# Kernel optimization log

Hardware: AMD Instinct MI355X
Metric: run time of the kernel (lower is better)

The kernel has to match this reference:

```python
import jax, jax.numpy as jnp
import numpy as np

F, H, D, A, B = 500, 2000, 64, 64, 4096


def setup_inputs() -> dict:
    key = jax.random.key(0)
    ks = jax.random.split(key, 6)
    values = jax.random.normal(ks[0], (B, F), dtype=jnp.float32)
    feat_emb = jax.random.normal(ks[1], (F, D), dtype=jnp.float32) * 0.02
    hid_emb = jax.random.normal(ks[2], (H, D), dtype=jnp.float32) * 0.02
    Ww = jax.random.normal(ks[3], (2 * D, A), dtype=jnp.float32) * (1.0 / np.sqrt(2 * D))
    bw = jnp.zeros((A,), dtype=jnp.float32)
    Wu = jax.random.normal(ks[4], (A, 1), dtype=jnp.float32) * (1.0 / np.sqrt(A))
    mask = jax.random.bernoulli(ks[5], 0.1, (F, F + H, 1))
    return {"values": values, "feat_emb": feat_emb, "hid_emb": hid_emb,
            "Ww": Ww, "bw": bw, "Wu": Wu, "mask": mask}


def reference(values, feat_emb, hid_emb, Ww, bw, Wu, mask):
    d = feat_emb.shape[1]
    # full embedding matrix: concat(feature, hidden) -> [F+H, d]
    full = jnp.concatenate([feat_emb, hid_emb], axis=0)
    # Dense(tanh) on concat([feat_emb tiled, full tiled], axis=2) == split-weight form:
    # avoids materializing the [F, F+H, 2d] concat tensor (same math).
    W1, W2 = Ww[:d], Ww[d:]
    pre_f = feat_emb @ W1          # [F, A]
    pre_w = full @ W2              # [F+H, A]
    h = jnp.tanh(pre_f[:, None, :] + pre_w[None, :, :] + bw)  # [F, F+H, A]
    score = h @ Wu                 # [F, F+H, 1]
    # masked exp-normalize (not a stable softmax: original uses raw exp)
    score = jnp.where(mask, jnp.exp(score), 0.0)
    ssum = jnp.sum(score, axis=1, keepdims=True)        # [F, 1, 1]
    ssum = jnp.where(ssum == 0, 1.0, ssum)
    attn = score / ssum                                  # [F, F+H, 1]
    context = jnp.sum(attn * full[None, :, :], axis=1)   # [F, d]
    return values @ context                              # [B, d]
```

## Files before the change

### kernel.cpp

```cpp
#include <hip/hip_runtime.h>
#include <cstdint>
#include <cstddef>

#define F_N 500
#define H_N 2000
#define JN  2500
#define D_N 64
#define A_N 64
#define B_N 4096

#define SPLIT  2
#define JCHUNK 1250

__global__ __launch_bounds__(256) void k_pre(
    const float* __restrict__ feat, const float* __restrict__ hid,
    const float* __restrict__ Ww,   const float* __restrict__ bw,
    float* __restrict__ pre_f, float* __restrict__ pre_w)
{
    const int lane = threadIdx.x & 63;
    const int wave = threadIdx.x >> 6;
    int row = blockIdx.x * 4 + wave;
    row = __builtin_amdgcn_readfirstlane(row);
    if (row >= F_N + JN) return;

    const float* emb;
    const float* W;
    float*       outp;
    float acc0, acc1 = 0.0f;

    if (row < F_N) {
        emb  = feat + (size_t)row * D_N;
        W    = Ww;
        outp = pre_f + (size_t)row * A_N;
        acc0 = bw[lane];
    } else {
        const int j = row - F_N;
        emb  = (j < F_N) ? (feat + (size_t)j * D_N)
                         : (hid + (size_t)(j - F_N) * D_N);
        W    = Ww + D_N * A_N;
        outp = pre_w + (size_t)j * A_N;
        acc0 = 0.0f;
    }

    #pragma unroll
    for (int d = 0; d < D_N; d += 2) {
        acc0 = fmaf(emb[d],     W[(d    ) * A_N + lane], acc0);
        acc1 = fmaf(emb[d + 1], W[(d + 1) * A_N + lane], acc1);
    }
    outp[lane] = acc0 + acc1;
}

__global__ __launch_bounds__(256, 8) void k_attn(
    const float* __restrict__ feat, const float* __restrict__ hid,
    const float* __restrict__ pre_f, const float* __restrict__ pre_w,
    const float* __restrict__ Wu,   const void* __restrict__ mask,
    float* __restrict__ csum, float* __restrict__ esum)
{
    const int tid  = threadIdx.x;
    const int lane = tid & 63;
    const int wave = tid >> 6;
    const int i    = blockIdx.x >> 1;
    const int sub  = blockIdx.x & 1;
    const int jbase = sub * JCHUNK;

    __shared__ int   list[JCHUNK];
    __shared__ float earr[JCHUNK];
    __shared__ float s_ctx[4][64];
    __shared__ int   nact;

    if (tid == 0) nact = 0;
    __syncthreads();

    const uint32_t* mw = (const uint32_t*)mask;
    const uint32_t probe = mw[lane] | mw[64 + lane] | mw[128 + lane] | mw[192 + lane];
    const bool byteMode = (__ballot(probe > 1u) != 0ull);

    const uint8_t*  mb = (const uint8_t*)mask + (size_t)i * JN + jbase;
    const uint32_t* mi = (const uint32_t*)mask + (size_t)i * JN + jbase;

    for (int t = tid; t < 1280; t += 256) {
        uint32_t m = 0;
        if (t < JCHUNK) m = byteMode ? (uint32_t)mb[t] : mi[t];
        const unsigned long long act = __ballot(m != 0);
        const int cnt = __popcll(act);
        int base = 0;
        if (lane == 0 && cnt) base = atomicAdd(&nact, cnt);
        base = __shfl(base, 0, 64);
        if (m) {
            const int rank = __popcll(act & ((1ull << lane) - 1ull));
            list[base + rank] = jbase + t;
        }
    }
    __syncthreads();
    const int n = nact;

    const float* pf = pre_f + (size_t)i * A_N;
    for (int idx = tid; idx < n; idx += 256) {
        const int j = list[idx];
        const float4* pwj = (const float4*)(pre_w + (size_t)j * A_N);
        float s0 = 0.0f, s1 = 0.0f, s2 = 0.0f, s3 = 0.0f;
        #pragma unroll
        for (int q = 0; q < 16; ++q) {
            const float4 v = pwj[q];
            const int a = q * 4;
            const float x0 = pf[a + 0] + v.x;
            const float x1 = pf[a + 1] + v.y;
            const float x2 = pf[a + 2] + v.z;
            const float x3 = pf[a + 3] + v.w;
            const float t0 = fmaf(-2.0f, __builtin_amdgcn_rcpf(__expf(2.0f * x0) + 1.0f), 1.0f);
            const float t1 = fmaf(-2.0f, __builtin_amdgcn_rcpf(__expf(2.0f * x1) + 1.0f), 1.0f);
            const float t2 = fmaf(-2.0f, __builtin_amdgcn_rcpf(__expf(2.0f * x2) + 1.0f), 1.0f);
            const float t3 = fmaf(-2.0f, __builtin_amdgcn_rcpf(__expf(2.0f * x3) + 1.0f), 1.0f);
            s0 = fmaf(Wu[a + 0], t0, s0);
            s1 = fmaf(Wu[a + 1], t1, s1);
            s2 = fmaf(Wu[a + 2], t2, s2);
            s3 = fmaf(Wu[a + 3], t3, s3);
        }
        earr[idx] = __expf((s0 + s1) + (s2 + s3));
    }
    __syncthreads();

    float cacc = 0.0f;
    int idx = wave;
    for (; idx + 12 < n; idx += 16) {
        const float e0 = earr[idx];      const int j0 = list[idx];
        const float e1 = earr[idx + 4];  const int j1 = list[idx + 4];
        const float e2 = earr[idx + 8];  const int j2 = list[idx + 8];
        const float e3 = earr[idx + 12]; const int j3 = list[idx + 12];
        const float* r0 = (j0 < F_N) ? (feat + (size_t)j0 * D_N) : (hid + (size_t)(j0 - F_N) * D_N);
        const float* r1 = (j1 < F_N) ? (feat + (size_t)j1 * D_N) : (hid + (size_t)(j1 - F_N) * D_N);
        const float* r2 = (j2 < F_N) ? (feat + (size_t)j2 * D_N) : (hid + (size_t)(j2 - F_N) * D_N);
        const float* r3 = (j3 < F_N) ? (feat + (size_t)j3 * D_N) : (hid + (size_t)(j3 - F_N) * D_N);
        const float v0 = r0[lane];
        const float v1 = r1[lane];
        const float v2 = r2[lane];
        const float v3 = r3[lane];
        cacc = fmaf(e0, v0, cacc);
        cacc = fmaf(e1, v1, cacc);
        cacc = fmaf(e2, v2, cacc);
        cacc = fmaf(e3, v3, cacc);
    }
    for (; idx < n; idx += 4) {
        const float e = earr[idx];
        const int   j = list[idx];
        const float* row = (j < F_N) ? (feat + (size_t)j * D_N)
                                     : (hid + (size_t)(j - F_N) * D_N);
        cacc = fmaf(e, row[lane], cacc);
    }
    s_ctx[wave][lane] = cacc;
    __syncthreads();

    if (wave == 0) {
        const float c4 = s_ctx[0][lane] + s_ctx[1][lane] + s_ctx[2][lane] + s_ctx[3][lane];
        float ss = 0.0f;
        for (int k = lane; k < n; k += 64) ss += earr[k];
        #pragma unroll
        for (int off = 1; off < 64; off <<= 1) ss += __shfl_xor(ss, off, 64);
        csum[((size_t)sub * F_N + i) * D_N + lane] = c4;
        if (lane == 0) esum[sub * F_N + i] = ss;
    }
}

__global__ __launch_bounds__(256) void k_out(
    const float* __restrict__ values, const float* __restrict__ csum,
    const float* __restrict__ esum,   float* __restrict__ out)
{
    const int tid  = threadIdx.x;
    const int lane = tid & 63;
    const int wave = tid >> 6;
    int r0 = blockIdx.x * 8 + wave * 2;
    r0 = __builtin_amdgcn_readfirstlane(r0);

    __shared__ float ctx_l[100 * 64];

    float4 cbuf0[7], cbuf1[7];
    float  ebuf[7];

    float acc0 = 0.0f, acc1 = 0.0f;

    {
        const float4* cp0 = (const float4*)csum;
        const float4* cp1 = (const float4*)(csum + (size_t)F_N * D_N);
        #pragma unroll
        for (int q = 0; q < 7; ++q) {
            const int t = tid + q * 256;
            if (t < 1600) {
                cbuf0[q] = cp0[t];
                cbuf1[q] = cp1[t];
                ebuf[q]  = esum[t >> 4] + esum[F_N + (t >> 4)];
            }
        }
    }

    for (int chunk = 0; chunk < 5; ++chunk) {
        __syncthreads();
        {
            float4* cl = (float4*)ctx_l;
            #pragma unroll
            for (int q = 0; q < 7; ++q) {
                const int t = tid + q * 256;
                if (t < 1600) {
                    const float e   = ebuf[q];
                    const float inv = (e == 0.0f) ? 1.0f : __builtin_amdgcn_rcpf(e);
                    float4 c;
                    c.x = (cbuf0[q].x + cbuf1[q].x) * inv;
                    c.y = (cbuf0[q].y + cbuf1[q].y) * inv;
                    c.z = (cbuf0[q].z + cbuf1[q].z) * inv;
                    c.w = (cbuf0[q].w + cbuf1[q].w) * inv;
                    cl[t] = c;
                }
            }
        }
        __syncthreads();

        if (chunk < 4) {
            const int k0n = (chunk + 1) * 100;
            const float4* cp0 = (const float4*)(csum + (size_t)k0n * 64);
            const float4* cp1 = (const float4*)(csum + (size_t)(F_N + k0n) * 64);
            #pragma unroll
            for (int q = 0; q < 7; ++q) {
                const int t = tid + q * 256;
                if (t < 1600) {
                    cbuf0[q] = cp0[t];
                    cbuf1[q] = cp1[t];
                    ebuf[q]  = esum[k0n + (t >> 4)] + esum[F_N + k0n + (t >> 4)];
                }
            }
        }

        const int k0 = chunk * 100;
        const float* v0 = values + (size_t)(r0 + 0) * 500 + k0;
        const float* v1 = values + (size_t)(r0 + 1) * 500 + k0;
        #pragma unroll 10
        for (int k = 0; k < 100; k += 4) {
            const float c0 = ctx_l[(k + 0) * 64 + lane];
            const float c1 = ctx_l[(k + 1) * 64 + lane];
            const float c2 = ctx_l[(k + 2) * 64 + lane];
            const float c3 = ctx_l[(k + 3) * 64 + lane];
            acc0 = fmaf(v0[k + 0], c0, acc0); acc0 = fmaf(v0[k + 1], c1, acc0);
            acc0 = fmaf(v0[k + 2], c2, acc0); acc0 = fmaf(v0[k + 3], c3, acc0);
            acc1 = fmaf(v1[k + 0], c0, acc1); acc1 = fmaf(v1[k + 1], c1, acc1);
            acc1 = fmaf(v1[k + 2], c2, acc1); acc1 = fmaf(v1[k + 3], c3, acc1);
        }
    }

    out[(size_t)(r0 + 0) * 64 + lane] = acc0;
    out[(size_t)(r0 + 1) * 64 + lane] = acc1;
}

extern "C" void kernel_launch(void* const* d_in, const int* in_sizes, int n_in,
                              void* d_out, int out_size, void* d_ws, size_t ws_size,
                              hipStream_t stream)
{
    const float* values = (const float*)d_in[0];
    const float* feat   = (const float*)d_in[1];
    const float* hid    = (const float*)d_in[2];
    const float* Ww     = (const float*)d_in[3];
    const float* bw     = (const float*)d_in[4];
    const float* Wu     = (const float*)d_in[5];
    const void*  mask   = d_in[6];
    float* out = (float*)d_out;

    float* wsf   = (float*)d_ws;
    float* pre_f = wsf;
    float* pre_w = wsf + 32000;
    float* csum  = wsf + 192000;
    float* esum  = wsf + 256000;

    k_pre <<<750,  256, 0, stream>>>(feat, hid, Ww, bw, pre_f, pre_w);
    k_attn<<<1000, 256, 0, stream>>>(feat, hid, pre_f, pre_w, Wu, mask, csum, esum);
    k_out <<<512,  256, 0, stream>>>(values, csum, esum, out);
}
```

Measured before the change: 113.6 us.

## Fuse pre-projection into attention kernel, recompute per-active-j projections per wave

Removes the separate k_pre launch and its pre_f/pre_w workspace. Each block now computes its own pre_f row and holds the W2 column in registers. For each active j, a wave computes the 64-wide projection on the fly, with one lane per attention unit, and reduces the score across lanes with shuffles. The exp-sum is accumulated per wave, so the final reduction pass over earr goes away. This trades one launch and a global round-trip for redundant projection work per (i,j) pair, higher register pressure (64-float array, occupancy hint lowered to 4), and a shuffle reduction per active element.

```diff
diff --git a/kernel.cpp b/kernel.cpp
--- a/kernel.cpp
+++ b/kernel.cpp
@@ -12,47 +12,9 @@
 #define SPLIT  2
 #define JCHUNK 1250
 
-__global__ __launch_bounds__(256) void k_pre(
+__global__ __launch_bounds__(256, 4) void k_attn_fused(
     const float* __restrict__ feat, const float* __restrict__ hid,
     const float* __restrict__ Ww,   const float* __restrict__ bw,
-    float* __restrict__ pre_f, float* __restrict__ pre_w)
-{
-    const int lane = threadIdx.x & 63;
-    const int wave = threadIdx.x >> 6;
-    int row = blockIdx.x * 4 + wave;
-    row = __builtin_amdgcn_readfirstlane(row);
-    if (row >= F_N + JN) return;
-
-    const float* emb;
-    const float* W;
-    float*       outp;
-    float acc0, acc1 = 0.0f;
-
-    if (row < F_N) {
-        emb  = feat + (size_t)row * D_N;
-        W    = Ww;
-        outp = pre_f + (size_t)row * A_N;
-        acc0 = bw[lane];
-    } else {
-        const int j = row - F_N;
-        emb  = (j < F_N) ? (feat + (size_t)j * D_N)
-                         : (hid + (size_t)(j - F_N) * D_N);
-        W    = Ww + D_N * A_N;
-        outp = pre_w + (size_t)j * A_N;
-        acc0 = 0.0f;
-    }
-
-    #pragma unroll
-    for (int d = 0; d < D_N; d += 2) {
-        acc0 = fmaf(emb[d],     W[(d    ) * A_N + lane], acc0);
-        acc1 = fmaf(emb[d + 1], W[(d + 1) * A_N + lane], acc1);
-    }
-    outp[lane] = acc0 + acc1;
-}
-
-__global__ __launch_bounds__(256, 8) void k_attn(
-    const float* __restrict__ feat, const float* __restrict__ hid,
-    const float* __restrict__ pre_f, const float* __restrict__ pre_w,
     const float* __restrict__ Wu,   const void* __restrict__ mask,
     float* __restrict__ csum, float* __restrict__ esum)
 {
@@ -66,9 +28,24 @@
     __shared__ int   list[JCHUNK];
     __shared__ float earr[JCHUNK];
     __shared__ float s_ctx[4][64];
+    __shared__ float s_ss[4];
     __shared__ int   nact;
 
     if (tid == 0) nact = 0;
+
+    const float wu = Wu[lane];
+    float w2c[64];
+    #pragma unroll
+    for (int d = 0; d < D_N; ++d)
+        w2c[d] = Ww[(size_t)(D_N + d) * A_N + lane];
+
+    float pf = bw[lane];
+    {
+        const float* fr = feat + (size_t)i * D_N;
+        #pragma unroll
+        for (int d = 0; d < D_N; ++d)
+            pf = fmaf(fr[d], Ww[(size_t)d * A_N + lane], pf);
+    }
     __syncthreads();
 
     const uint32_t* mw = (const uint32_t*)mask;
@@ -94,30 +71,36 @@
     __syncthreads();
     const int n = nact;
 
-    const float* pf = pre_f + (size_t)i * A_N;
-    for (int idx = tid; idx < n; idx += 256) {
-        const int j = list[idx];
-        const float4* pwj = (const float4*)(pre_w + (size_t)j * A_N);
-        float s0 = 0.0f, s1 = 0.0f, s2 = 0.0f, s3 = 0.0f;
-        #pragma unroll
-        for (int q = 0; q < 16; ++q) {
-            const float4 v = pwj[q];
-            const int a = q * 4;
-            const float x0 = pf[a + 0] + v.x;
-            const float x1 = pf[a + 1] + v.y;
-            const float x2 = pf[a + 2] + v.z;
-            const float x3 = pf[a + 3] + v.w;
-            const float t0 = fmaf(-2.0f, __builtin_amdgcn_rcpf(__expf(2.0f * x0) + 1.0f), 1.0f);
-            const float t1 = fmaf(-2.0f, __builtin_amdgcn_rcpf(__expf(2.0f * x1) + 1.0f), 1.0f);
-            const float t2 = fmaf(-2.0f, __builtin_amdgcn_rcpf(__expf(2.0f * x2) + 1.0f), 1.0f);
-            const float t3 = fmaf(-2.0f, __builtin_amdgcn_rcpf(__expf(2.0f * x3) + 1.0f), 1.0f);
-            s0 = fmaf(Wu[a + 0], t0, s0);
-            s1 = fmaf(Wu[a + 1], t1, s1);
-            s2 = fmaf(Wu[a + 2], t2, s2);
-            s3 = fmaf(Wu[a + 3], t3, s3);
-        }
-        earr[idx] = __expf((s0 + s1) + (s2 + s3));
-    }
+    float ss_w = 0.0f;
+    for (int pos = wave; pos < n; pos += 4) {
+        const int j = __builtin_amdgcn_readfirstlane(list[pos]);
+        const float* row = (j < F_N) ? (feat + (size_t)j * D_N)
+                                     : (hid + (size_t)(j - F_N) * D_N);
+        const float4* r4 = (const float4*)row;
+        float x0 = pf, x1 = 0.0f;
+        #pragma unroll
+        for (int q = 0; q < 16; q += 2) {
+            const float4 va = r4[q];
+            const float4 vb = r4[q + 1];
+            x0 = fmaf(va.x, w2c[4 * q + 0], x0);
+            x0 = fmaf(va.y, w2c[4 * q + 1], x0);
+            x0 = fmaf(va.z, w2c[4 * q + 2], x0);
+            x0 = fmaf(va.w, w2c[4 * q + 3], x0);
+            x1 = fmaf(vb.x, w2c[4 * q + 4], x1);
+            x1 = fmaf(vb.y, w2c[4 * q + 5], x1);
+            x1 = fmaf(vb.z, w2c[4 * q + 6], x1);
+            x1 = fmaf(vb.w, w2c[4 * q + 7], x1);
+        }
+        const float x = x0 + x1;
+        const float t = fmaf(-2.0f, __builtin_amdgcn_rcpf(__expf(2.0f * x) + 1.0f), 1.0f);
+        float m = wu * t;
+        #pragma unroll
+        for (int off = 1; off < 64; off <<= 1) m += __shfl_xor(m, off, 64);
+        const float e = __expf(m);
+        if (lane == 0) earr[pos] = e;
+        ss_w += e;
+    }
+    if (lane == 0) s_ss[wave] = ss_w;
     __syncthreads();
 
     float cacc = 0.0f;
@@ -152,10 +135,7 @@
 
     if (wave == 0) {
         const float c4 = s_ctx[0][lane] + s_ctx[1][lane] + s_ctx[2][lane] + s_ctx[3][lane];
-        float ss = 0.0f;
-        for (int k = lane; k < n; k += 64) ss += earr[k];
-        #pragma unroll
-        for (int off = 1; off < 64; off <<= 1) ss += __shfl_xor(ss, off, 64);
+        const float ss = s_ss[0] + s_ss[1] + s_ss[2] + s_ss[3];
         csum[((size_t)sub * F_N + i) * D_N + lane] = c4;
         if (lane == 0) esum[sub * F_N + i] = ss;
     }
@@ -261,13 +241,10 @@
     const void*  mask   = d_in[6];
     float* out = (float*)d_out;
 
-    float* wsf   = (float*)d_ws;
-    float* pre_f = wsf;
-    float* pre_w = wsf + 32000;
-    float* csum  = wsf + 192000;
-    float* esum  = wsf + 256000;
-
-    k_pre <<<750,  256, 0, stream>>>(feat, hid, Ww, bw, pre_f, pre_w);
-    k_attn<<<1000, 256, 0, stream>>>(feat, hid, pre_f, pre_w, Wu, mask, csum, esum);
-    k_out <<<512,  256, 0, stream>>>(values, csum, esum, out);
+    float* wsf  = (float*)d_ws;
+    float* csum = wsf;
+    float* esum = wsf + 64000;
+
+    k_attn_fused<<<1000, 256, 0, stream>>>(feat, hid, Ww, bw, Wu, mask, csum, esum);
+    k_out       <<<512,  256, 0, stream>>>(values, csum, esum, out);
 }
```

New measurement: 150.4 us. 32.4% more time.

## Fuse attention and output kernels using a software grid barrier

Applied to the files above, without the earlier changes.

Merges the attention and output-GEMM kernels into one persistent launch. Every block signals an atomic counter after writing its partial context sums, and the first 512 blocks spin-wait on a flag before running the values×context product. While they wait, those blocks touch their rows of `values` to pull them into cache. This removes one kernel launch boundary and its tail, but it relies on all 1000 blocks being co-resident: occupancy is capped at 4 blocks per CU and LDS is shared through a union. If that residency assumption fails, the spin barrier could deadlock.

```diff
diff --git a/kernel.cpp b/kernel.cpp
--- a/kernel.cpp
+++ b/kernel.cpp
@@ -11,12 +11,16 @@
 
 #define SPLIT  2
 #define JCHUNK 1250
+#define NBLK   1000
 
 __global__ __launch_bounds__(256) void k_pre(
     const float* __restrict__ feat, const float* __restrict__ hid,
     const float* __restrict__ Ww,   const float* __restrict__ bw,
-    float* __restrict__ pre_f, float* __restrict__ pre_w)
+    float* __restrict__ pre_f, float* __restrict__ pre_w,
+    int* __restrict__ bar)
 {
+    if (blockIdx.x == 0 && threadIdx.x < 2) bar[threadIdx.x] = 0;
+
     const int lane = threadIdx.x & 63;
     const int wave = threadIdx.x >> 6;
     int row = blockIdx.x * 4 + wave;
@@ -50,202 +54,240 @@
     outp[lane] = acc0 + acc1;
 }
 
-__global__ __launch_bounds__(256, 8) void k_attn(
+__global__ __launch_bounds__(256, 4) void k_fused2(
     const float* __restrict__ feat, const float* __restrict__ hid,
     const float* __restrict__ pre_f, const float* __restrict__ pre_w,
     const float* __restrict__ Wu,   const void* __restrict__ mask,
-    float* __restrict__ csum, float* __restrict__ esum)
+    const float* __restrict__ values,
+    float* __restrict__ csum, float* __restrict__ esum,
+    float* __restrict__ out,  int* __restrict__ bar)
 {
     const int tid  = threadIdx.x;
     const int lane = tid & 63;
     const int wave = tid >> 6;
-    const int i    = blockIdx.x >> 1;
-    const int sub  = blockIdx.x & 1;
-    const int jbase = sub * JCHUNK;
-
-    __shared__ int   list[JCHUNK];
-    __shared__ float earr[JCHUNK];
-    __shared__ float s_ctx[4][64];
+
+    __shared__ __align__(16) char smem[25600];
+    __shared__ float s_ss[4];
     __shared__ int   nact;
 
-    if (tid == 0) nact = 0;
+    {
+        int*   list = (int*)smem;
+        float* earr = (float*)(smem + 5120);
+        float (*s_ctx)[64] = (float (*)[64])(smem + 10240);
+
+        const int i     = blockIdx.x >> 1;
+        const int sub   = blockIdx.x & 1;
+        const int jbase = sub * JCHUNK;
+
+        if (tid == 0) nact = 0;
+        __syncthreads();
+
+        const uint32_t* mw = (const uint32_t*)mask;
+        const uint32_t probe = mw[lane] | mw[64 + lane] | mw[128 + lane] | mw[192 + lane];
+        const bool byteMode = (__ballot(probe > 1u) != 0ull);
+
+        const uint8_t*  mb = (const uint8_t*)mask + (size_t)i * JN + jbase;
+        const uint32_t* mi = (const uint32_t*)mask + (size_t)i * JN + jbase;
+
+        for (int t = tid; t < 1280; t += 256) {
+            uint32_t m = 0;
+            if (t < JCHUNK) m = byteMode ? (uint32_t)mb[t] : mi[t];
+            const unsigned long long act = __ballot(m != 0);
+            const int cnt = __popcll(act);
+            int base = 0;
+            if (lane == 0 && cnt) base = atomicAdd(&nact, cnt);
+            base = __shfl(base, 0, 64);
+            if (m) {
+                const int rank = __popcll(act & ((1ull << lane) - 1ull));
+                list[base + rank] = jbase + t;
+            }
+        }
+        __syncthreads();
+        const int n = nact;
+
+        const float* pf = pre_f + (size_t)i * A_N;
+        for (int idx = tid; idx < n; idx += 256) {
+            const int j = list[idx];
+            const float4* pwj = (const float4*)(pre_w + (size_t)j * A_N);
+            float s0 = 0.0f, s1 = 0.0f, s2 = 0.0f, s3 = 0.0f;
+            #pragma unroll
+            for (int q = 0; q < 16; ++q) {
+                const float4 v = pwj[q];
+                const int a = q * 4;
+                const float x0 = pf[a + 0] + v.x;
+                const float x1 = pf[a + 1] + v.y;
+                const float x2 = pf[a + 2] + v.z;
+                const float x3 = pf[a + 3] + v.w;
+                const float t0 = fmaf(-2.0f, __builtin_amdgcn_rcpf(__expf(2.0f * x0) + 1.0f), 1.0f);
+                const float t1 = fmaf(-2.0f, __builtin_amdgcn_rcpf(__expf(2.0f * x1) + 1.0f), 1.0f);
+                const float t2 = fmaf(-2.0f, __builtin_amdgcn_rcpf(__expf(2.0f * x2) + 1.0f), 1.0f);
+                const float t3 = fmaf(-2.0f, __builtin_amdgcn_rcpf(__expf(2.0f * x3) + 1.0f), 1.0f);
+                s0 = fmaf(Wu[a + 0], t0, s0);
+                s1 = fmaf(Wu[a + 1], t1, s1);
+                s2 = fmaf(Wu[a + 2], t2, s2);
+                s3 = fmaf(Wu[a + 3], t3, s3);
+            }
+            earr[idx] = __expf((s0 + s1) + (s2 + s3));
+        }
+        __syncthreads();
+
+        float cacc = 0.0f;
+        int idx = wave;
+        for (; idx + 12 < n; idx += 16) {
+            const float e0 = earr[idx];      const int j0 = list[idx];
+            const float e1 = earr[idx + 4];  const int j1 = list[idx + 4];
+            const float e2 = earr[idx + 8];  const int j2 = list[idx + 8];
+            const float e3 = earr[idx + 12]; const int j3 = list[idx + 12];
+            const float* r0 = (j0 < F_N) ? (feat + (size_t)j0 * D_N) : (hid + (size_t)(j0 - F_N) * D_N);
+            const float* r1 = (j1 < F_N) ? (feat + (size_t)j1 * D_N) : (hid + (size_t)(j1 - F_N) * D_N);
+            const float* r2 = (j2 < F_N) ? (feat + (size_t)j2 * D_N) : (hid + (size_t)(j2 - F_N) * D_N);
+            const float* r3 = (j3 < F_N) ? (feat + (size_t)j3 * D_N) : (hid + (size_t)(j3 - F_N) * D_N);
+            const float v0 = r0[lane];
+            const float v1 = r1[lane];
+            const float v2 = r2[lane];
+            const float v3 = r3[lane];
+            cacc = fmaf(e0, v0, cacc);
+            cacc = fmaf(e1, v1, cacc);
+            cacc = fmaf(e2, v2, cacc);
+            cacc = fmaf(e3, v3, cacc);
+        }
+        for (; idx < n; idx += 4) {
+            const float e = earr[idx];
+            const int   j = list[idx];
+            const float* row = (j < F_N) ? (feat + (size_t)j * D_N)
+                                         : (hid + (size_t)(j - F_N) * D_N);
+            cacc = fmaf(e, row[lane], cacc);
+        }
+        s_ctx[wave][lane] = cacc;
+        __syncthreads();
+
+        if (wave == 0) {
+            const float c4 = s_ctx[0][lane] + s_ctx[1][lane] + s_ctx[2][lane] + s_ctx[3][lane];
+            float ss = 0.0f;
+            for (int k = lane; k < n; k += 64) ss += earr[k];
+            #pragma unroll
+            for (int off = 1; off < 64; off <<= 1) ss += __shfl_xor(ss, off, 64);
+            csum[((size_t)sub * F_N + i) * D_N + lane] = c4;
+            if (lane == 0) esum[sub * F_N + i] = ss;
+        }
+    }
+
+    const bool doOut = (blockIdx.x < 512);
+    const int  rowB  = blockIdx.x * 8;
+
     __syncthreads();
-
-    const uint32_t* mw = (const uint32_t*)mask;
-    const uint32_t probe = mw[lane] | mw[64 + lane] | mw[128 + lane] | mw[192 + lane];
-    const bool byteMode = (__ballot(probe > 1u) != 0ull);
-
-    const uint8_t*  mb = (const uint8_t*)mask + (size_t)i * JN + jbase;
-    const uint32_t* mi = (const uint32_t*)mask + (size_t)i * JN + jbase;
-
-    for (int t = tid; t < 1280; t += 256) {
-        uint32_t m = 0;
-        if (t < JCHUNK) m = byteMode ? (uint32_t)mb[t] : mi[t];
-        const unsigned long long act = __ballot(m != 0);
-        const int cnt = __popcll(act);
-        int base = 0;
-        if (lane == 0 && cnt) base = atomicAdd(&nact, cnt);
-        base = __shfl(base, 0, 64);
-        if (m) {
-            const int rank = __popcll(act & ((1ull << lane) - 1ull));
-            list[base + rank] = jbase + t;
-        }
+    if (tid == 0) {
+        __threadfence();
+        const int old = __hip_atomic_fetch_add(bar + 0, 1, __ATOMIC_ACQ_REL,
+                                               __HIP_MEMORY_SCOPE_AGENT);
+        if (old == NBLK - 1)
+            __hip_atomic_store(bar + 1, 1, __ATOMIC_RELEASE,
+                               __HIP_MEMORY_SCOPE_AGENT);
+    }
+    if (!doOut) return;
+
+    float warm = 0.0f;
+    {
+        const float4* vp = (const float4*)(values + (size_t)rowB * 500);
+        #pragma unroll
+        for (int q = 0; q < 4; ++q) {
+            const int t = tid + q * 256;
+            if (t < 1000) warm += vp[t].x;
+        }
+    }
+    asm volatile("" :: "v"(warm));
+
+    if (tid == 0) {
+        while (__hip_atomic_load(bar + 1, __ATOMIC_RELAXED,
+                                 __HIP_MEMORY_SCOPE_AGENT) == 0) {
+            __builtin_amdgcn_s_sleep(32);
+        }
+        const int v = __hip_atomic_load(bar + 1, __ATOMIC_ACQUIRE,
+                                        __HIP_MEMORY_SCOPE_AGENT);
+        if (v == 0) __builtin_amdgcn_s_sleep(1);
     }
     __syncthreads();
-    const int n = nact;
-
-    const float* pf = pre_f + (size_t)i * A_N;
-    for (int idx = tid; idx < n; idx += 256) {
-        const int j = list[idx];
-        const float4* pwj = (const float4*)(pre_w + (size_t)j * A_N);
-        float s0 = 0.0f, s1 = 0.0f, s2 = 0.0f, s3 = 0.0f;
-        #pragma unroll
-        for (int q = 0; q < 16; ++q) {
-            const float4 v = pwj[q];
-            const int a = q * 4;
-            const float x0 = pf[a + 0] + v.x;
-            const float x1 = pf[a + 1] + v.y;
-            const float x2 = pf[a + 2] + v.z;
-            const float x3 = pf[a + 3] + v.w;
-            const float t0 = fmaf(-2.0f, __builtin_amdgcn_rcpf(__expf(2.0f * x0) + 1.0f), 1.0f);
-            const float t1 = fmaf(-2.0f, __builtin_amdgcn_rcpf(__expf(2.0f * x1) + 1.0f), 1.0f);
-            const float t2 = fmaf(-2.0f, __builtin_amdgcn_rcpf(__expf(2.0f * x2) + 1.0f), 1.0f);
-            const float t3 = fmaf(-2.0f, __builtin_amdgcn_rcpf(__expf(2.0f * x3) + 1.0f), 1.0f);
-            s0 = fmaf(Wu[a + 0], t0, s0);
-            s1 = fmaf(Wu[a + 1], t1, s1);
-            s2 = fmaf(Wu[a + 2], t2, s2);
-            s3 = fmaf(Wu[a + 3], t3, s3);
-        }
-        earr[idx] = __expf((s0 + s1) + (s2 + s3));
-    }
-    __syncthreads();
-
-    float cacc = 0.0f;
-    int idx = wave;
-    for (; idx + 12 < n; idx += 16) {
-        const float e0 = earr[idx];      const int j0 = list[idx];
-        const float e1 = earr[idx + 4];  const int j1 = list[idx + 4];
-        const float e2 = earr[idx + 8];  const int j2 = list[idx + 8];
-        const float e3 = earr[idx + 12]; const int j3 = list[idx + 12];
-        const float* r0 = (j0 < F_N) ? (feat + (size_t)j0 * D_N) : (hid + (size_t)(j0 - F_N) * D_N);
-        const float* r1 = (j1 < F_N) ? (feat + (size_t)j1 * D_N) : (hid + (size_t)(j1 - F_N) * D_N);
-        const float* r2 = (j2 < F_N) ? (feat + (size_t)j2 * D_N) : (hid + (size_t)(j2 - F_N) * D_N);
-        const float* r3 = (j3 < F_N) ? (feat + (size_t)j3 * D_N) : (hid + (size_t)(j3 - F_N) * D_N);
-        const float v0 = r0[lane];
-        const float v1 = r1[lane];
-        const float v2 = r2[lane];
-        const float v3 = r3[lane];
-        cacc = fmaf(e0, v0, cacc);
-        cacc = fmaf(e1, v1, cacc);
-        cacc = fmaf(e2, v2, cacc);
-        cacc = fmaf(e3, v3, cacc);
-    }
-    for (; idx < n; idx += 4) {
-        const float e = earr[idx];
-        const int   j = list[idx];
-        const float* row = (j < F_N) ? (feat + (size_t)j * D_N)
-                                     : (hid + (size_t)(j - F_N) * D_N);
-        cacc = fmaf(e, row[lane], cacc);
-    }
-    s_ctx[wave][lane] = cacc;
-    __syncthreads();
-
-    if (wave == 0) {
-        const float c4 = s_ctx[0][lane] + s_ctx[1][lane] + s_ctx[2][lane] + s_ctx[3][lane];
-        float ss = 0.0f;
-        for (int k = lane; k < n; k += 64) ss += earr[k];
-        #pragma unroll
-        for (int off = 1; off < 64; off <<= 1) ss += __shfl_xor(ss, off, 64);
-        csum[((size_t)sub * F_N + i) * D_N + lane] = c4;
-        if (lane == 0) esum[sub * F_N + i] = ss;
-    }
-}
-
-__global__ __launch_bounds__(256) void k_out(
-    const float* __restrict__ values, const float* __restrict__ csum,
-    const float* __restrict__ esum,   float* __restrict__ out)
-{
-    const int tid  = threadIdx.x;
-    const int lane = tid & 63;
-    const int wave = tid >> 6;
-    int r0 = blockIdx.x * 8 + wave * 2;
-    r0 = __builtin_amdgcn_readfirstlane(r0);
-
-    __shared__ float ctx_l[100 * 64];
-
-    float4 cbuf0[7], cbuf1[7];
-    float  ebuf[7];
-
-    float acc0 = 0.0f, acc1 = 0.0f;
 
     {
-        const float4* cp0 = (const float4*)csum;
-        const float4* cp1 = (const float4*)(csum + (size_t)F_N * D_N);
-        #pragma unroll
-        for (int q = 0; q < 7; ++q) {
-            const int t = tid + q * 256;
-            if (t < 1600) {
-                cbuf0[q] = cp0[t];
-                cbuf1[q] = cp1[t];
-                ebuf[q]  = esum[t >> 4] + esum[F_N + (t >> 4)];
-            }
-        }
-    }
-
-    for (int chunk = 0; chunk < 5; ++chunk) {
-        __syncthreads();
+        float* ctx_l = (float*)smem;
+
+        int r0 = rowB + wave * 2;
+        r0 = __builtin_amdgcn_readfirstlane(r0);
+
+        float4 cbuf0[7], cbuf1[7];
+        float  ebuf[7];
+
+        float acc0 = 0.0f, acc1 = 0.0f;
+
         {
-            float4* cl = (float4*)ctx_l;
-            #pragma unroll
-            for (int q = 0; q < 7; ++q) {
-                const int t = tid + q * 256;
-                if (t < 1600) {
-                    const float e   = ebuf[q];
-                    const float inv = (e == 0.0f) ? 1.0f : __builtin_amdgcn_rcpf(e);
-                    float4 c;
-                    c.x = (cbuf0[q].x + cbuf1[q].x) * inv;
-                    c.y = (cbuf0[q].y + cbuf1[q].y) * inv;
-                    c.z = (cbuf0[q].z + cbuf1[q].z) * inv;
-                    c.w = (cbuf0[q].w + cbuf1[q].w) * inv;
-                    cl[t] = c;
-                }
-            }
-        }
-        __syncthreads();
-
-        if (chunk < 4) {
-            const int k0n = (chunk + 1) * 100;
-            const float4* cp0 = (const float4*)(csum + (size_t)k0n * 64);
-            const float4* cp1 = (const float4*)(csum + (size_t)(F_N + k0n) * 64);
+            const float4* cp0 = (const float4*)csum;
+            const float4* cp1 = (const float4*)(csum + (size_t)F_N * D_N);
             #pragma unroll
             for (int q = 0; q < 7; ++q) {
                 const int t = tid + q * 256;
                 if (t < 1600) {
                     cbuf0[q] = cp0[t];
                     cbuf1[q] = cp1[t];
-                    ebuf[q]  = esum[k0n + (t >> 4)] + esum[F_N + k0n + (t >> 4)];
+                    ebuf[q]  = esum[t >> 4] + esum[F_N + (t >> 4)];
                 }
             }
         }
 
-        const int k0 = chunk * 100;
-        const float* v0 = values + (size_t)(r0 + 0) * 500 + k0;
-        const float* v1 = values + (size_t)(r0 + 1) * 500 + k0;
-        #pragma unroll 10
-        for (int k = 0; k < 100; k += 4) {
-            const float c0 = ctx_l[(k + 0) * 64 + lane];
-            const float c1 = ctx_l[(k + 1) * 64 + lane];
-            const float c2 = ctx_l[(k + 2) * 64 + lane];
-            const float c3 = ctx_l[(k + 3) * 64 + lane];
-            acc0 = fmaf(v0[k + 0], c0, acc0); acc0 = fmaf(v0[k + 1], c1, acc0);
-            acc0 = fmaf(v0[k + 2], c2, acc0); acc0 = fmaf(v0[k + 3], c3, acc0);
-            acc1 = fmaf(v1[k + 0], c0, acc1); acc1 = fmaf(v1[k + 1], c1, acc1);
-            acc1 = fmaf(v1[k + 2], c2, acc1); acc1 = fmaf(v1[k + 3], c3, acc1);
-        }
-    }
-
-    out[(size_t)(r0 + 0) * 64 + lane] = acc0;
-    out[(size_t)(r0 + 1) * 64 + lane] = acc1;
+        for (int chunk = 0; chunk < 5; ++chunk) {
+            __syncthreads();
+            {
+                float4* cl = (float4*)ctx_l;
+                #pragma unroll
+                for (int q = 0; q < 7; ++q) {
+                    const int t = tid + q * 256;
+                    if (t < 1600) {
+                        const float e   = ebuf[q];
+                        const float inv = (e == 0.0f) ? 1.0f : __builtin_amdgcn_rcpf(e);
+                        float4 c;
+                        c.x = (cbuf0[q].x + cbuf1[q].x) * inv;
+                        c.y = (cbuf0[q].y + cbuf1[q].y) * inv;
+                        c.z = (cbuf0[q].z + cbuf1[q].z) * inv;
+                        c.w = (cbuf0[q].w + cbuf1[q].w) * inv;
+                        cl[t] = c;
+                    }
+                }
+            }
+            __syncthreads();
+
+            if (chunk < 4) {
+                const int k0n = (chunk + 1) * 100;
+                const float4* cp0 = (const float4*)(csum + (size_t)k0n * 64);
+                const float4* cp1 = (const float4*)(csum + (size_t)(F_N + k0n) * 64);
+                #pragma unroll
+                for (int q = 0; q < 7; ++q) {
+                    const int t = tid + q * 256;
+                    if (t < 1600) {
+                        cbuf0[q] = cp0[t];
+                        cbuf1[q] = cp1[t];
+                        ebuf[q]  = esum[k0n + (t >> 4)] + esum[F_N + k0n + (t >> 4)];
+                    }
+                }
+            }
+
+            const int k0 = chunk * 100;
+            const float* v0 = values + (size_t)(r0 + 0) * 500 + k0;
+            const float* v1 = values + (size_t)(r0 + 1) * 500 + k0;
+            #pragma unroll 10
+            for (int k = 0; k < 100; k += 4) {
+                const float c0 = ctx_l[(k + 0) * 64 + lane];
+                const float c1 = ctx_l[(k + 1) * 64 + lane];
+                const float c2 = ctx_l[(k + 2) * 64 + lane];
+                const float c3 = ctx_l[(k + 3) * 64 + lane];
+                acc0 = fmaf(v0[k + 0], c0, acc0); acc0 = fmaf(v0[k + 1], c1, acc0);
+                acc0 = fmaf(v0[k + 2], c2, acc0); acc0 = fmaf(v0[k + 3], c3, acc0);
+                acc1 = fmaf(v1[k + 0], c0, acc1); acc1 = fmaf(v1[k + 1], c1, acc1);
+                acc1 = fmaf(v1[k + 2], c2, acc1); acc1 = fmaf(v1[k + 3], c3, acc1);
+            }
+        }
+
+        out[(size_t)(r0 + 0) * 64 + lane] = acc0;
+        out[(size_t)(r0 + 1) * 64 + lane] = acc1;
+    }
 }
 
 extern "C" void kernel_launch(void* const* d_in, const int* in_sizes, int n_in,
@@ -266,8 +308,9 @@
     float* pre_w = wsf + 32000;
     float* csum  = wsf + 192000;
     float* esum  = wsf + 256000;
-
-    k_pre <<<750,  256, 0, stream>>>(feat, hid, Ww, bw, pre_f, pre_w);
-    k_attn<<<1000, 256, 0, stream>>>(feat, hid, pre_f, pre_w, Wu, mask, csum, esum);
-    k_out <<<512,  256, 0, stream>>>(values, csum, esum, out);
+    int*   bar   = (int*)(wsf + 257000);
+
+    k_pre   <<<750,  256, 0, stream>>>(feat, hid, Ww, bw, pre_f, pre_w, bar);
+    k_fused2<<<NBLK, 256, 0, stream>>>(feat, hid, pre_f, pre_w, Wu, mask,
+                                       values, csum, esum, out, bar);
 }
```

New measurement: 201.6 us. +77.4%, slower.
